# Kernel optimization log

Measured on AMD Instinct MI355X. Metric: run time of the kernel, lower is better.

Reference implementation:

```python
import jax, jax.numpy as jnp
import numpy as np

WS = 7          # window_size
HEADS = 3
HD = 32         # head_dim
HIDDEN = 96
DISP = WS // 2  # 3
NEG_INF = float('-inf')


def _relative_indices():
    idx = np.array([[i, j] for i in range(WS) for j in range(WS)])
    rel = idx[None, :, :] - idx[:, None, :] + WS - 1  # [49,49,2], values in [0, 2*WS-2]
    return rel.astype(np.int32)


def _upper_lower_mask():
    m = np.zeros((WS * WS, WS * WS), dtype=np.float32)
    m[-DISP * WS:, :-DISP * WS] = NEG_INF
    m[:-DISP * WS, -DISP * WS:] = NEG_INF
    return m


def setup_inputs() -> dict:
    key = jax.random.key(0)
    ks = jax.random.split(key, 6)
    B, H, W = 32, 56, 56
    inner = HEADS * HD
    return {
        'x': jax.random.normal(ks[0], (B, H, W, HIDDEN), jnp.float32),
        'w_qkv': jax.random.normal(ks[1], (HIDDEN, inner * 3), jnp.float32) * 0.05,
        'b_qkv': jax.random.normal(ks[2], (inner * 3,), jnp.float32) * 0.05,
        'pos_embedding': jax.random.normal(ks[3], (2 * WS - 1, 2 * WS - 1), jnp.float32),
        'w_out': jax.random.normal(ks[4], (inner, HIDDEN), jnp.float32) * 0.05,
        'b_out': jax.random.normal(ks[5], (HIDDEN,), jnp.float32) * 0.05,
    }


def reference(x, w_qkv, b_qkv, pos_embedding, w_out, b_out):
    B, H, W, _ = x.shape
    nw_h, nw_w = H // WS, W // WS
    nw = nw_h * nw_w
    scale = HIDDEN ** (-0.5)  # original scales by hidden_dim**-0.5

    rel = jnp.asarray(_relative_indices())
    ul_mask = jnp.asarray(_upper_lower_mask())

    # cyclic shift
    xs = jnp.roll(x, (-DISP, -DISP), axis=(1, 2))
    qkv = xs @ w_qkv + b_qkv
    q, k, v = jnp.split(qkv, 3, axis=-1)

    def to_windows(e):
        # [B,H,W,heads*hd] -> [B,heads,nw,WS*WS,hd]
        e = e.reshape(B, nw_h, WS, nw_w, WS, HEADS, HD)
        e = e.transpose(0, 5, 1, 3, 2, 4, 6)
        return e.reshape(B, HEADS, nw, WS * WS, HD)

    q, k, v = to_windows(q), to_windows(k), to_windows(v)

    att = jnp.einsum('bhwid,bhwjd->bhwij', q, k) * scale
    att = att + pos_embedding[rel[:, :, 0], rel[:, :, 1]]
    # shifted: original only adds upper_lower_mask (right_left line is a no-op bug)
    att = att.at[:, :, -nw_w:].add(ul_mask)
    att = jax.nn.softmax(att, axis=-1)

    out = jnp.einsum('bhwij,bhwjd->bhwid', att, v)
    out = out.reshape(B, HEADS, nw_h, nw_w, WS, WS, HD)
    out = out.transpose(0, 2, 4, 3, 5, 1, 6).reshape(B, H, W, HEADS * HD)
    out = out @ w_out + b_out
    out = jnp.roll(out, (DISP, DISP), axis=(1, 2))
    return out
```

## Files before the change

### kernel.cpp

```cpp
#include <hip/hip_runtime.h>
#include <hip/hip_bf16.h>

using bf16 = __hip_bfloat16;
typedef __attribute__((ext_vector_type(8))) short short8;
typedef __attribute__((ext_vector_type(4))) float floatx4;

#define B_      32
#define HH      56
#define WW      56
#define HIDDEN  96
#define HEADS   3
#define HD      32
#define WS_     7
#define DISP    3
#define NWH     8
#define NWW     8
#define NW      64
#define WS2     49
#define NFRAG_QKV (3*6*3*64)
#define NFRAG_OUT (6*3*64)

__global__ __launch_bounds__(256) void prep_weights_kernel(
    const float* __restrict__ w_qkv, const float* __restrict__ w_out,
    bf16* __restrict__ wfq, bf16* __restrict__ wfo) {
  int f = blockIdx.x * 256 + threadIdx.x;
  if (f < NFRAG_QKV) {
    int lane = f & 63, t = f >> 6;
    int kb = t % 3, t2 = t / 3, c6 = t2 % 6, ci = t2 / 6;
    int col = ci * 96 + c6 * 16 + (lane & 15);
    int k0 = kb * 32 + (lane >> 4) * 8;
    bf16 vals[8];
#pragma unroll
    for (int j = 0; j < 8; j++) vals[j] = __float2bfloat16(w_qkv[(k0 + j) * 288 + col]);
    *(short8*)&wfq[(size_t)f * 8] = *(const short8*)vals;
  } else if (f < NFRAG_QKV + NFRAG_OUT) {
    int fo = f - NFRAG_QKV;
    int lane = fo & 63, t = fo >> 6;
    int kb = t % 3, c6 = t / 3;
    int col = c6 * 16 + (lane & 15);
    int k0 = kb * 32 + (lane >> 4) * 8;
    bf16 vals[8];
#pragma unroll
    for (int j = 0; j < 8; j++) vals[j] = __float2bfloat16(w_out[(k0 + j) * 96 + col]);
    *(short8*)&wfo[(size_t)fo * 8] = *(const short8*)vals;
  }
}

__device__ inline unsigned short bf16_bits(float f) {
  unsigned u = __float_as_uint(f);
  unsigned r = u + 0x7fffu + ((u >> 16) & 1u);
  return (unsigned short)(r >> 16);
}

__global__ __launch_bounds__(256, 3) void fused_swin_kernel(
    const float* __restrict__ x,
    const bf16* __restrict__ wfq, const bf16* __restrict__ wfo,
    const float* __restrict__ b_qkv, const float* __restrict__ b_out,
    const float* __restrict__ pos_emb, float* __restrict__ out) {

  __shared__ unsigned short slabA[3][64][40];
  __shared__ unsigned short slabB[3][64][40];
  __shared__ unsigned short vT[3][32][72];
  __shared__ unsigned short es[64][72];

  const int blk = blockIdx.x;
  const int nw = blk & 63, b = blk >> 6;
  const int wy = nw >> 3, wx = nw & 7;
  const int tid = threadIdx.x;
  const int lane = tid & 63, wv = tid >> 6;
  const int n_ = lane & 15, quad = lane >> 4;

  const short8* wfQ = (const short8*)wfq;
  short8 wcur0 = wfQ[(size_t)((wv * 3 + 0) * 64 + lane)];
  short8 wcur1 = wfQ[(size_t)((wv * 3 + 1) * 64 + lane)];
  short8 wcur2 = wfQ[(size_t)((wv * 3 + 2) * 64 + lane)];

  {
    const int rowp = tid >> 2, s0 = tid & 3;
    const bool haveRow = rowp < WS2;
    const float* xrow = x;
    if (haveRow) {
      const int py = rowp / WS_, px = rowp % WS_;
      int h = wy * WS_ + py + DISP; if (h >= HH) h -= HH;
      int w = wx * WS_ + px + DISP; if (w >= WW) w -= WW;
      xrow = &x[((size_t)(b * HH + h) * WW + w) * HIDDEN];
    }
#pragma unroll
    for (int p = 0; p < 6; p++) {
      const int seg = s0 + 4 * p;
      const int kb = seg >> 3, c4 = (seg & 7) << 2;
      ushort4 pk = (ushort4){0, 0, 0, 0};
      if (haveRow) {
        const float4 xv = *(const float4*)&xrow[seg * 4];
        pk.x = bf16_bits(xv.x); pk.y = bf16_bits(xv.y);
        pk.z = bf16_bits(xv.z); pk.w = bf16_bits(xv.w);
      }
      *(ushort4*)&slabA[kb][rowp][c4] = pk;
    }
  }

  const bool maskedw = (nw >= NW - NWW);
  const int i0 = 16 * wv + 4 * quad;
  float pelv[4][4];
#pragma unroll
  for (int r = 0; r < 4; r++) {
    const int i_r = i0 + r;
    const int iy = i_r / WS_, ix = i_r % WS_;
#pragma unroll
    for (int jt = 0; jt < 4; jt++) {
      const int j = 16 * jt + n_;
      const int jy = j / WS_, jx = j % WS_;
      int idx = (jy - iy + 6) * 13 + (jx - ix + 6);
      idx = idx < 0 ? 0 : (idx > 168 ? 168 : idx);
      const bool live = (j < WS2) && (i_r < WS2) &&
                        !(maskedw && ((i_r >= 28) != (j >= 28)));
      pelv[r][jt] = live ? pos_emb[idx] : -1e30f;
    }
  }
  __syncthreads();

  short8 af[4][3];
#pragma unroll
  for (int m = 0; m < 4; m++)
#pragma unroll
    for (int kb = 0; kb < 3; kb++)
      af[m][kb] = *(const short8*)&slabA[kb][16 * m + n_][quad * 8];
  __syncthreads();

  {
    int t = wv;
    while (t < 18) {
      const int tn = t + 4;
      short8 wn0 = wcur0, wn1 = wcur1, wn2 = wcur2;
      if (tn < 18) {
        wn0 = wfQ[(size_t)((tn * 3 + 0) * 64 + lane)];
        wn1 = wfQ[(size_t)((tn * 3 + 1) * 64 + lane)];
        wn2 = wfQ[(size_t)((tn * 3 + 2) * 64 + lane)];
      }
      const int ci = t / 6, c6 = t % 6, head = c6 >> 1;
      floatx4 acc[4];
      if (ci < 2) {
        const float4 bq = *(const float4*)&b_qkv[t * 16 + 4 * quad];
#pragma unroll
        for (int m = 0; m < 4; m++) acc[m] = (floatx4){bq.x, bq.y, bq.z, bq.w};
#pragma unroll
        for (int m = 0; m < 4; m++) {
          acc[m] = __builtin_amdgcn_mfma_f32_16x16x32_bf16(wcur0, af[m][0], acc[m], 0, 0, 0);
          acc[m] = __builtin_amdgcn_mfma_f32_16x16x32_bf16(wcur1, af[m][1], acc[m], 0, 0, 0);
          acc[m] = __builtin_amdgcn_mfma_f32_16x16x32_bf16(wcur2, af[m][2], acc[m], 0, 0, 0);
        }
        unsigned short (*tgt)[64][40] = (ci == 0) ? slabA : slabB;
        const int dc0 = ((c6 & 1) << 4) + 4 * quad;
#pragma unroll
        for (int m = 0; m < 4; m++) {
          ushort4 pk;
          pk.x = bf16_bits(acc[m][0]); pk.y = bf16_bits(acc[m][1]);
          pk.z = bf16_bits(acc[m][2]); pk.w = bf16_bits(acc[m][3]);
          *(ushort4*)&tgt[head][16 * m + n_][dc0] = pk;
        }
      } else {
        const float bias = b_qkv[t * 16 + n_];
#pragma unroll
        for (int m = 0; m < 4; m++) acc[m] = (floatx4){bias, bias, bias, bias};
#pragma unroll
        for (int m = 0; m < 4; m++) {
          acc[m] = __builtin_amdgcn_mfma_f32_16x16x32_bf16(af[m][0], wcur0, acc[m], 0, 0, 0);
          acc[m] = __builtin_amdgcn_mfma_f32_16x16x32_bf16(af[m][1], wcur1, acc[m], 0, 0, 0);
          acc[m] = __builtin_amdgcn_mfma_f32_16x16x32_bf16(af[m][2], wcur2, acc[m], 0, 0, 0);
        }
        const int dc = ((c6 & 1) << 4) + n_;
#pragma unroll
        for (int m = 0; m < 4; m++) {
          ushort4 pk;
          pk.x = bf16_bits(acc[m][0]); pk.y = bf16_bits(acc[m][1]);
          pk.z = bf16_bits(acc[m][2]); pk.w = bf16_bits(acc[m][3]);
          *(ushort4*)&vT[head][dc][16 * m + 4 * quad] = pk;
        }
      }
      wcur0 = wn0; wcur1 = wn1; wcur2 = wn2;
      t = tn;
    }
  }
  __syncthreads();

  const float scale = 0.10206207261596575f;
  const floatx4 zero4 = (floatx4){0.f, 0.f, 0.f, 0.f};
#pragma unroll
  for (int h = 0; h < HEADS; h++) {
    const short8 aq = *(const short8*)&slabA[h][16 * wv + n_][quad * 8];
    floatx4 sAcc[4];
#pragma unroll
    for (int jt = 0; jt < 4; jt++) {
      const short8 bk = *(const short8*)&slabB[h][16 * jt + n_][quad * 8];
      sAcc[jt] = __builtin_amdgcn_mfma_f32_16x16x32_bf16(aq, bk, zero4, 0, 0, 0);
    }

    float ei[4][4], rowsum[4];
#pragma unroll
    for (int r = 0; r < 4; r++) {
      rowsum[r] = 0.f;
#pragma unroll
      for (int jt = 0; jt < 4; jt++) {
        const float e = __expf(fmaf(sAcc[jt][r], scale, pelv[r][jt]));
        ei[r][jt] = e;
        rowsum[r] += e;
      }
    }
#pragma unroll
    for (int r = 0; r < 4; r++) {
      float s = rowsum[r];
      s += __shfl_xor(s, 1); s += __shfl_xor(s, 2);
      s += __shfl_xor(s, 4); s += __shfl_xor(s, 8);
      const float inv = s > 0.f ? 1.0f / s : 0.f;
#pragma unroll
      for (int jt = 0; jt < 4; jt++)
        es[i0 + r][16 * jt + n_] = bf16_bits(ei[r][jt] * inv);
    }

    short8 ap[2];
#pragma unroll
    for (int kc = 0; kc < 2; kc++)
      ap[kc] = *(const short8*)&es[16 * wv + n_][32 * kc + quad * 8];
    floatx4 oAcc[2] = {zero4, zero4};
#pragma unroll
    for (int nt = 0; nt < 2; nt++)
#pragma unroll
      for (int kc = 0; kc < 2; kc++) {
        const short8 bv = *(const short8*)&vT[h][16 * nt + n_][32 * kc + quad * 8];
        oAcc[nt] = __builtin_amdgcn_mfma_f32_16x16x32_bf16(bv, ap[kc], oAcc[nt], 0, 0, 0);
      }
#pragma unroll
    for (int nt = 0; nt < 2; nt++) {
      ushort4 pk;
      pk.x = bf16_bits(oAcc[nt][0]); pk.y = bf16_bits(oAcc[nt][1]);
      pk.z = bf16_bits(oAcc[nt][2]); pk.w = bf16_bits(oAcc[nt][3]);
      *(ushort4*)&slabA[h][16 * wv + n_][16 * nt + 4 * quad] = pk;
    }
  }
  __syncthreads();

  short8 af2[4][3];
#pragma unroll
  for (int m = 0; m < 4; m++)
#pragma unroll
    for (int kb = 0; kb < 3; kb++)
      af2[m][kb] = *(const short8*)&slabA[kb][16 * m + n_][quad * 8];

  unsigned obase[4][4];
#pragma unroll
  for (int m = 0; m < 4; m++)
#pragma unroll
    for (int r = 0; r < 4; r++) {
      const int row = 16 * m + 4 * quad + r;
      const int py = row / WS_, px = row % WS_;
      int hg = wy * WS_ + py + DISP; if (hg >= HH) hg -= HH;
      int wg = wx * WS_ + px + DISP; if (wg >= WW) wg -= WW;
      obase[m][r] = (unsigned)(((b * HH + hg) * WW + wg) * HIDDEN + n_);
    }

  const short8* wfO = (const short8*)wfo;
  {
    int t = wv;
    short8 oc0 = wfO[(size_t)((t * 3 + 0) * 64 + lane)];
    short8 oc1 = wfO[(size_t)((t * 3 + 1) * 64 + lane)];
    short8 oc2 = wfO[(size_t)((t * 3 + 2) * 64 + lane)];
    while (t < 6) {
      const int tn = t + 4;
      short8 on0 = oc0, on1 = oc1, on2 = oc2;
      if (tn < 6) {
        on0 = wfO[(size_t)((tn * 3 + 0) * 64 + lane)];
        on1 = wfO[(size_t)((tn * 3 + 1) * 64 + lane)];
        on2 = wfO[(size_t)((tn * 3 + 2) * 64 + lane)];
      }
      const float bias = b_out[t * 16 + n_];
      floatx4 acc[4];
#pragma unroll
      for (int m = 0; m < 4; m++) acc[m] = (floatx4){bias, bias, bias, bias};
#pragma unroll
      for (int m = 0; m < 4; m++) {
        acc[m] = __builtin_amdgcn_mfma_f32_16x16x32_bf16(af2[m][0], oc0, acc[m], 0, 0, 0);
        acc[m] = __builtin_amdgcn_mfma_f32_16x16x32_bf16(af2[m][1], oc1, acc[m], 0, 0, 0);
        acc[m] = __builtin_amdgcn_mfma_f32_16x16x32_bf16(af2[m][2], oc2, acc[m], 0, 0, 0);
      }
#pragma unroll
      for (int m = 0; m < 4; m++)
#pragma unroll
        for (int r = 0; r < 4; r++) {
          if (16 * m + 4 * quad + r < WS2)
            out[(size_t)obase[m][r] + t * 16] = acc[m][r];
        }
      oc0 = on0; oc1 = on1; oc2 = on2;
      t = tn;
    }
  }
}

extern "C" void kernel_launch(void* const* d_in, const int* in_sizes, int n_in,
                              void* d_out, int out_size, void* d_ws, size_t ws_size,
                              hipStream_t stream) {
  const float* x     = (const float*)d_in[0];
  const float* w_qkv = (const float*)d_in[1];
  const float* b_qkv = (const float*)d_in[2];
  const float* pos   = (const float*)d_in[3];
  const float* w_out = (const float*)d_in[4];
  const float* b_out = (const float*)d_in[5];
  float* out = (float*)d_out;

  bf16* wfq = (bf16*)d_ws;
  bf16* wfo = wfq + (size_t)NFRAG_QKV * 8;

  prep_weights_kernel<<<18, 256, 0, stream>>>(w_qkv, w_out, wfq, wfo);
  fused_swin_kernel<<<B_ * NW, 256, 0, stream>>>(x, wfq, wfo, b_qkv, b_out, pos, out);
}
```

Baseline: 129.1 us.

## Keep softmax probabilities in registers and precompute position-bias tables

The score MFMA is transposed so each lane holds one query row's probabilities in the exact layout the PV MFMA needs as an operand. This removes the `es` shared-memory round trip and the 16-lane row-sum shuffles, and normalization is deferred to the output. K rows are stored permuted to match that layout. The position-bias plus mask table is precomputed once in the prep kernel and read as float4, the slab padding is dropped to cut LDS, and launch bounds are raised to 4 blocks per CU. Risks: bank conflicts from the unpadded slabs and register pressure at the higher occupancy target.

```diff
diff --git a/kernel.cpp b/kernel.cpp
--- a/kernel.cpp
+++ b/kernel.cpp
@@ -19,10 +19,21 @@
 #define WS2     49
 #define NFRAG_QKV (3*6*3*64)
 #define NFRAG_OUT (6*3*64)
-
-__global__ __launch_bounds__(256) void prep_weights_kernel(
+#define NPEL      (2*64*64)
+
+__device__ inline unsigned short bf16_bits(float f) {
+  unsigned u = __float_as_uint(f);
+  unsigned r = u + 0x7fffu + ((u >> 16) & 1u);
+  return (unsigned short)(r >> 16);
+}
+__device__ inline unsigned packbf(float lo, float hi) {
+  return (unsigned)bf16_bits(lo) | ((unsigned)bf16_bits(hi) << 16);
+}
+
+__global__ __launch_bounds__(256) void prep_kernel(
     const float* __restrict__ w_qkv, const float* __restrict__ w_out,
-    bf16* __restrict__ wfq, bf16* __restrict__ wfo) {
+    const float* __restrict__ pos_emb,
+    bf16* __restrict__ wfq, bf16* __restrict__ wfo, float* __restrict__ pelT) {
   int f = blockIdx.x * 256 + threadIdx.x;
   if (f < NFRAG_QKV) {
     int lane = f & 63, t = f >> 6;
@@ -43,25 +54,28 @@
 #pragma unroll
     for (int j = 0; j < 8; j++) vals[j] = __float2bfloat16(w_out[(k0 + j) * 96 + col]);
     *(short8*)&wfo[(size_t)fo * 8] = *(const short8*)vals;
-  }
-}
-
-__device__ inline unsigned short bf16_bits(float f) {
-  unsigned u = __float_as_uint(f);
-  unsigned r = u + 0x7fffu + ((u >> 16) & 1u);
-  return (unsigned short)(r >> 16);
-}
-
-__global__ __launch_bounds__(256, 3) void fused_swin_kernel(
+  } else {
+    int p = f - (NFRAG_QKV + NFRAG_OUT);
+    if (p < NPEL) {
+      int mk = p >> 12, i = (p >> 6) & 63, j = p & 63;
+      int iy = i / WS_, ix = i % WS_, jy = j / WS_, jx = j % WS_;
+      int idx = (jy - iy + 6) * 13 + (jx - ix + 6);
+      idx = idx < 0 ? 0 : (idx > 168 ? 168 : idx);
+      bool live = (i < WS2) && (j < WS2) && !(mk && ((i >= 28) != (j >= 28)));
+      pelT[p] = live ? pos_emb[idx] : -1e30f;
+    }
+  }
+}
+
+__global__ __launch_bounds__(256, 4) void fused_swin_kernel(
     const float* __restrict__ x,
     const bf16* __restrict__ wfq, const bf16* __restrict__ wfo,
     const float* __restrict__ b_qkv, const float* __restrict__ b_out,
-    const float* __restrict__ pos_emb, float* __restrict__ out) {
-
-  __shared__ unsigned short slabA[3][64][40];
-  __shared__ unsigned short slabB[3][64][40];
+    const float* __restrict__ pelT, float* __restrict__ out) {
+
+  __shared__ unsigned short slabA[3][64][32];
+  __shared__ unsigned short slabB[3][64][32];
   __shared__ unsigned short vT[3][32][72];
-  __shared__ unsigned short es[64][72];
 
   const int blk = blockIdx.x;
   const int nw = blk & 63, b = blk >> 6;
@@ -89,32 +103,25 @@
     for (int p = 0; p < 6; p++) {
       const int seg = s0 + 4 * p;
       const int kb = seg >> 3, c4 = (seg & 7) << 2;
-      ushort4 pk = (ushort4){0, 0, 0, 0};
+      uint2 pk = (uint2){0u, 0u};
       if (haveRow) {
         const float4 xv = *(const float4*)&xrow[seg * 4];
-        pk.x = bf16_bits(xv.x); pk.y = bf16_bits(xv.y);
-        pk.z = bf16_bits(xv.z); pk.w = bf16_bits(xv.w);
-      }
-      *(ushort4*)&slabA[kb][rowp][c4] = pk;
+        pk.x = packbf(xv.x, xv.y);
+        pk.y = packbf(xv.z, xv.w);
+      }
+      *(uint2*)&slabA[kb][rowp][c4] = pk;
     }
   }
 
   const bool maskedw = (nw >= NW - NWW);
-  const int i0 = 16 * wv + 4 * quad;
   float pelv[4][4];
-#pragma unroll
-  for (int r = 0; r < 4; r++) {
-    const int i_r = i0 + r;
-    const int iy = i_r / WS_, ix = i_r % WS_;
+  {
+    const float4* pt4 = (const float4*)&pelT[(maskedw ? 4096 : 0) + (16 * wv + n_) * 64];
 #pragma unroll
     for (int jt = 0; jt < 4; jt++) {
-      const int j = 16 * jt + n_;
-      const int jy = j / WS_, jx = j % WS_;
-      int idx = (jy - iy + 6) * 13 + (jx - ix + 6);
-      idx = idx < 0 ? 0 : (idx > 168 ? 168 : idx);
-      const bool live = (j < WS2) && (i_r < WS2) &&
-                        !(maskedw && ((i_r >= 28) != (j >= 28)));
-      pelv[r][jt] = live ? pos_emb[idx] : -1e30f;
+      const float4 p4 = pt4[8 * (jt & 1) + (jt >> 1) + 2 * quad];
+      pelv[jt][0] = p4.x; pelv[jt][1] = p4.y;
+      pelv[jt][2] = p4.z; pelv[jt][3] = p4.w;
     }
   }
   __syncthreads();
@@ -128,6 +135,7 @@
   __syncthreads();
 
   {
+    const int rB = 32 * ((n_ >> 2) & 1) + 4 * (n_ >> 3) + (n_ & 3);
     int t = wv;
     while (t < 18) {
       const int tn = t + 4;
@@ -149,14 +157,23 @@
           acc[m] = __builtin_amdgcn_mfma_f32_16x16x32_bf16(wcur1, af[m][1], acc[m], 0, 0, 0);
           acc[m] = __builtin_amdgcn_mfma_f32_16x16x32_bf16(wcur2, af[m][2], acc[m], 0, 0, 0);
         }
-        unsigned short (*tgt)[64][40] = (ci == 0) ? slabA : slabB;
         const int dc0 = ((c6 & 1) << 4) + 4 * quad;
-#pragma unroll
-        for (int m = 0; m < 4; m++) {
-          ushort4 pk;
-          pk.x = bf16_bits(acc[m][0]); pk.y = bf16_bits(acc[m][1]);
-          pk.z = bf16_bits(acc[m][2]); pk.w = bf16_bits(acc[m][3]);
-          *(ushort4*)&tgt[head][16 * m + n_][dc0] = pk;
+        if (ci == 0) {
+#pragma unroll
+          for (int m = 0; m < 4; m++) {
+            uint2 st;
+            st.x = packbf(acc[m][0], acc[m][1]);
+            st.y = packbf(acc[m][2], acc[m][3]);
+            *(uint2*)&slabA[head][16 * m + n_][dc0] = st;
+          }
+        } else {
+#pragma unroll
+          for (int m = 0; m < 4; m++) {
+            uint2 st;
+            st.x = packbf(acc[m][0], acc[m][1]);
+            st.y = packbf(acc[m][2], acc[m][3]);
+            *(uint2*)&slabB[head][rB + 8 * m][dc0] = st;
+          }
         }
       } else {
         const float bias = b_qkv[t * 16 + n_];
@@ -171,10 +188,10 @@
         const int dc = ((c6 & 1) << 4) + n_;
 #pragma unroll
         for (int m = 0; m < 4; m++) {
-          ushort4 pk;
-          pk.x = bf16_bits(acc[m][0]); pk.y = bf16_bits(acc[m][1]);
-          pk.z = bf16_bits(acc[m][2]); pk.w = bf16_bits(acc[m][3]);
-          *(ushort4*)&vT[head][dc][16 * m + 4 * quad] = pk;
+          uint2 st;
+          st.x = packbf(acc[m][0], acc[m][1]);
+          st.y = packbf(acc[m][2], acc[m][3]);
+          *(uint2*)&vT[head][dc][16 * m + 4 * quad] = st;
         }
       }
       wcur0 = wn0; wcur1 = wn1; wcur2 = wn2;
@@ -192,49 +209,54 @@
 #pragma unroll
     for (int jt = 0; jt < 4; jt++) {
       const short8 bk = *(const short8*)&slabB[h][16 * jt + n_][quad * 8];
-      sAcc[jt] = __builtin_amdgcn_mfma_f32_16x16x32_bf16(aq, bk, zero4, 0, 0, 0);
-    }
-
-    float ei[4][4], rowsum[4];
-#pragma unroll
-    for (int r = 0; r < 4; r++) {
-      rowsum[r] = 0.f;
-#pragma unroll
-      for (int jt = 0; jt < 4; jt++) {
-        const float e = __expf(fmaf(sAcc[jt][r], scale, pelv[r][jt]));
-        ei[r][jt] = e;
-        rowsum[r] += e;
-      }
-    }
-#pragma unroll
-    for (int r = 0; r < 4; r++) {
-      float s = rowsum[r];
-      s += __shfl_xor(s, 1); s += __shfl_xor(s, 2);
-      s += __shfl_xor(s, 4); s += __shfl_xor(s, 8);
-      const float inv = s > 0.f ? 1.0f / s : 0.f;
-#pragma unroll
-      for (int jt = 0; jt < 4; jt++)
-        es[i0 + r][16 * jt + n_] = bf16_bits(ei[r][jt] * inv);
-    }
-
-    short8 ap[2];
-#pragma unroll
-    for (int kc = 0; kc < 2; kc++)
-      ap[kc] = *(const short8*)&es[16 * wv + n_][32 * kc + quad * 8];
+      sAcc[jt] = __builtin_amdgcn_mfma_f32_16x16x32_bf16(bk, aq, zero4, 0, 0, 0);
+    }
+
+    float ei[4][4];
+    float s = 0.f;
+#pragma unroll
+    for (int jt = 0; jt < 4; jt++)
+#pragma unroll
+      for (int r = 0; r < 4; r++) {
+        const float e = __expf(fmaf(sAcc[jt][r], scale, pelv[jt][r]));
+        ei[jt][r] = e;
+        s += e;
+      }
+    s += __shfl_xor(s, 16);
+    s += __shfl_xor(s, 32);
+    const float invq = s > 0.f ? 1.0f / s : 0.f;
+
+    unsigned pk2[4][2];
+#pragma unroll
+    for (int jt = 0; jt < 4; jt++) {
+      pk2[jt][0] = packbf(ei[jt][0], ei[jt][1]);
+      pk2[jt][1] = packbf(ei[jt][2], ei[jt][3]);
+    }
+    short8 apf[2];
+#pragma unroll
+    for (int kc = 0; kc < 2; kc++) {
+      union { unsigned u[4]; short8 s8; } fu;
+      fu.u[0] = pk2[kc][0];
+      fu.u[1] = pk2[kc][1];
+      fu.u[2] = pk2[2 + kc][0];
+      fu.u[3] = pk2[2 + kc][1];
+      apf[kc] = fu.s8;
+    }
+
     floatx4 oAcc[2] = {zero4, zero4};
 #pragma unroll
     for (int nt = 0; nt < 2; nt++)
 #pragma unroll
       for (int kc = 0; kc < 2; kc++) {
         const short8 bv = *(const short8*)&vT[h][16 * nt + n_][32 * kc + quad * 8];
-        oAcc[nt] = __builtin_amdgcn_mfma_f32_16x16x32_bf16(bv, ap[kc], oAcc[nt], 0, 0, 0);
+        oAcc[nt] = __builtin_amdgcn_mfma_f32_16x16x32_bf16(bv, apf[kc], oAcc[nt], 0, 0, 0);
       }
 #pragma unroll
     for (int nt = 0; nt < 2; nt++) {
-      ushort4 pk;
-      pk.x = bf16_bits(oAcc[nt][0]); pk.y = bf16_bits(oAcc[nt][1]);
-      pk.z = bf16_bits(oAcc[nt][2]); pk.w = bf16_bits(oAcc[nt][3]);
-      *(ushort4*)&slabA[h][16 * wv + n_][16 * nt + 4 * quad] = pk;
+      uint2 st;
+      st.x = packbf(oAcc[nt][0] * invq, oAcc[nt][1] * invq);
+      st.y = packbf(oAcc[nt][2] * invq, oAcc[nt][3] * invq);
+      *(uint2*)&slabA[h][16 * wv + n_][16 * nt + 4 * quad] = st;
     }
   }
   __syncthreads();
@@ -308,7 +330,8 @@
 
   bf16* wfq = (bf16*)d_ws;
   bf16* wfo = wfq + (size_t)NFRAG_QKV * 8;
-
-  prep_weights_kernel<<<18, 256, 0, stream>>>(w_qkv, w_out, wfq, wfo);
-  fused_swin_kernel<<<B_ * NW, 256, 0, stream>>>(x, wfq, wfo, b_qkv, b_out, pos, out);
-}
+  float* pelT = (float*)((char*)d_ws + (size_t)(NFRAG_QKV + NFRAG_OUT) * 8 * 2);
+
+  prep_kernel<<<50, 256, 0, stream>>>(w_qkv, w_out, pos, wfq, wfo, pelT);
+  fused_swin_kernel<<<B_ * NW, 256, 0, stream>>>(x, wfq, wfo, b_qkv, b_out, pelT, out);
+}
```

Result: faster. 126.5 us (-2.0%).
